# Performance work log

Measured on AMD Instinct MI355X. Metric: run time of the kernel, lower is better.

## Reference

```python
import jax, jax.numpy as jnp
import numpy as np

N_NODES, N_EDGES, N_FEAT, N_CLASSES = 100000, 1600000, 50, 40
K_HOPS = 2


def setup_inputs() -> dict:
    key = jax.random.key(0)
    k1, k2, k3 = jax.random.split(key, 3)
    x = jax.random.normal(k1, (N_NODES, N_FEAT), dtype=jnp.float32)
    edge_index = jax.random.randint(k2, (2, N_EDGES), 0, N_NODES, dtype=jnp.int64)
    # Linear(num_features -> num_classes) params (PyG stores [out,in]; we use [in,out])
    W = jax.random.normal(k3, (N_FEAT, N_CLASSES), dtype=jnp.float32) * 0.05
    b = jnp.zeros((N_CLASSES,), dtype=jnp.float32)
    return {"x": x, "edge_index": edge_index, "W": W, "b": b}


def reference(x, edge_index, W, b):
    N = x.shape[0]
    # gcn_norm: add self-loops, symmetric normalization D^-1/2 (A+I) D^-1/2
    loop = jnp.arange(N, dtype=edge_index.dtype)
    row = jnp.concatenate([edge_index[0], loop])  # source nodes
    col = jnp.concatenate([edge_index[1], loop])  # target nodes
    deg = jax.ops.segment_sum(jnp.ones(row.shape[0], x.dtype), col, num_segments=N)
    deg_inv_sqrt = jnp.where(deg > 0, jax.lax.rsqrt(deg), 0.0)
    norm = deg_inv_sqrt[row] * deg_inv_sqrt[col]  # [E+N]

    # K-hop propagation: h <- scatter_add(norm * h[row] -> col)
    h = x
    for _ in range(K_HOPS):
        h = jax.ops.segment_sum(norm[:, None] * h[row], col, num_segments=N)

    logits = h @ W + b  # [N, C]
    return jax.nn.log_softmax(logits, axis=1)
```

## Files before the change

kernel.cpp:

```cpp
#include <hip/hip_runtime.h>
#include <hip/hip_fp16.h>
#include <math.h>

#define NFEAT 50
#define NCLS 40
#define TPBK 256
#define TPBK_SHIFT 8
#define EPB 4096
#define MAXNB 512
#define CAP 8192

__device__ __forceinline__ __half2 u2h2(unsigned u) { return *(__half2*)&u; }
__device__ __forceinline__ unsigned h22u(__half2 h) { return *(unsigned*)&h; }
__device__ __forceinline__ __half2 shx_h2(__half2 v, int m) {
    int i = *(int*)&v; i = __shfl_xor(i, m); return *(__half2*)&i;
}


__global__ __launch_bounds__(1024) void k_bhist(const int* __restrict__ col, int E,
                                                int* __restrict__ hist, int NB) {
    __shared__ int h[MAXNB];
    for (int i = threadIdx.x; i < NB; i += 1024) h[i] = 0;
    __syncthreads();
    int i0 = blockIdx.x * EPB;
    #pragma unroll
    for (int k = 0; k < EPB / 1024; k++) {
        int e = i0 + k * 1024 + threadIdx.x;
        if (e < E) atomicAdd(&h[col[e] >> TPBK_SHIFT], 1);
    }
    __syncthreads();
    int* row = hist + (size_t)blockIdx.x * NB;
    for (int i = threadIdx.x; i < NB; i += 1024) row[i] = h[i];
}


__global__ __launch_bounds__(1024) void k_colscan(int* __restrict__ hist,
                                                  int* __restrict__ btot,
                                                  int NB, int PE) {
    int b = (blockIdx.x * 1024 + threadIdx.x) >> 6;
    int lane = threadIdx.x & 63;
    if (b >= NB) return;
    int carry = b * CAP;
    for (int c = 0; c < PE; c += 64) {
        int p = c + lane;
        int v = (p < PE) ? hist[(size_t)p * NB + b] : 0;
        int incl = v;
        #pragma unroll
        for (int d = 1; d < 64; d <<= 1) {
            int tmp = __shfl_up(incl, d);
            if (lane >= d) incl += tmp;
        }
        if (p < PE) hist[(size_t)p * NB + b] = carry + incl - v;
        carry += __shfl(incl, 63);
    }
    if (lane == 0) btot[b] = carry - b * CAP;
}


__global__ __launch_bounds__(1024) void k_part(const int* __restrict__ ei, int E,
                                               const int* __restrict__ hist,
                                               unsigned* __restrict__ pairs, int NB) {
    __shared__ int h[MAXNB];
    __shared__ int base[MAXNB];
    int t = threadIdx.x;
    const int* brow = hist + (size_t)blockIdx.x * NB;
    for (int i = t; i < NB; i += 1024) { h[i] = 0; base[i] = brow[i]; }
    __syncthreads();
    int i0 = blockIdx.x * EPB;
    int r[EPB / 1024], c[EPB / 1024];
    #pragma unroll
    for (int k = 0; k < EPB / 1024; k++) {
        int e = i0 + k * 1024 + t;
        if (e < E) {
            r[k] = ei[e];
            c[k] = ei[E + e];
        } else c[k] = -1;
    }
    #pragma unroll
    for (int k = 0; k < EPB / 1024; k++) {
        if (c[k] >= 0) {
            int bkt = c[k] >> TPBK_SHIFT;
            int p = base[bkt] + atomicAdd(&h[bkt], 1);
            pairs[p] = ((unsigned)r[k] << 8) | ((unsigned)c[k] & 255u);
        }
    }
}


__global__ __launch_bounds__(1024) void k_bucket(const unsigned* __restrict__ pairs,
                         const int* __restrict__ btot, int* __restrict__ rows,
                         int* __restrict__ cnt, int* __restrict__ offs,
                         float* __restrict__ dis, const float* __restrict__ x,
                         unsigned short* __restrict__ xb, int N) {
    int b = blockIdx.x;
    int ebeg = b * CAP, m = btot[b];
    int t0 = b << TPBK_SHIFT;
    __shared__ int h[TPBK];
    __shared__ int off[TPBK];
    __shared__ float diss[TPBK];
    __shared__ int wtot[4];
    int t = threadIdx.x;
    if (t < TPBK) h[t] = 0;
    __syncthreads();

    unsigned pc[4]; bool ok[4];
    #pragma unroll
    for (int k = 0; k < 4; k++) {
        int i = t + k * 1024;
        ok[k] = i < m;
        if (ok[k]) {
            pc[k] = pairs[ebeg + i];
            atomicAdd(&h[pc[k] & 255u], 1);
        }
    }
    for (int i = 4096 + t; i < m; i += 1024)
        atomicAdd(&h[pairs[ebeg + i] & 255u], 1);
    __syncthreads();

    int v = 0, incl = 0;
    if (t < TPBK) {
        v = h[t];
        h[t] = 0;
        incl = v;
        int l = t & 63;
        #pragma unroll
        for (int d = 1; d < 64; d <<= 1) {
            int tmp = __shfl_up(incl, d);
            if (l >= d) incl += tmp;
        }
        if (l == 63) wtot[t >> 6] = incl;
    }
    __syncthreads();
    if (t < TPBK) {
        int pre = 0;
        #pragma unroll
        for (int w = 0; w < 3; w++) if ((t >> 6) > w) pre += wtot[w];
        int excl = pre + incl - v;
        off[t] = excl;
        int tg = t0 + t;
        float d = rsqrtf((float)(v + 1));
        diss[t] = d;
        if (tg < N) {
            cnt[tg] = v;
            offs[tg] = ebeg + excl;
            dis[tg] = d;
        }
    }
    __syncthreads();

    #pragma unroll
    for (int k = 0; k < 4; k++) {
        if (ok[k]) {
            int lt = pc[k] & 255u;
            int pos = off[lt] + atomicAdd(&h[lt], 1);
            rows[ebeg + pos] = pc[k] >> 8;
        }
    }
    for (int i = 4096 + t; i < m; i += 1024) {
        unsigned p = pairs[ebeg + i];
        int lt = p & 255u;
        int pos = off[lt] + atomicAdd(&h[lt], 1);
        rows[ebeg + pos] = p >> 8;
    }

    int nmax = N - t0; if (nmax > TPBK) nmax = TPBK;
    for (int idx = t; idx < (nmax << 6); idx += 1024) {
        int nl = idx >> 6, f = idx & 63;
        int n = t0 + nl;
        float val = (f < NFEAT) ? x[(size_t)n * NFEAT + f] * diss[nl] : 0.f;
        __half hv = __float2half_rn(val);
        xb[((size_t)n << 6) + f] = *(unsigned short*)&hv;
    }
}


__global__ void k_prop(const unsigned short* __restrict__ zin, unsigned short* __restrict__ zout,
                       const float* __restrict__ dis, const int* __restrict__ offs,
                       const int* __restrict__ cnt, const int* __restrict__ rows, int N) {
    int wid = (blockIdx.x * blockDim.x + threadIdx.x) >> 6;
    int lane = threadIdx.x & 63;
    if (wid >= N) return;
    int g = lane >> 3;
    unsigned fl = (lane & 7) << 3;
    int beg = offs[wid], num = cnt[wid];

    uint4 sv = *(const uint4*)&zin[((unsigned)wid << 6) + fl];
    __half2 a0 = u2h2(g == 0 ? sv.x : 0u);
    __half2 a1 = u2h2(g == 0 ? sv.y : 0u);
    __half2 a2 = u2h2(g == 0 ? sv.z : 0u);
    __half2 a3 = u2h2(g == 0 ? sv.w : 0u);

    int full = num & ~31;
    int j = 0;
    for (; j < full; j += 32) {
        unsigned i0 = (unsigned)(beg + j) + (unsigned)g;
        int r0 = rows[i0], r1 = rows[i0 + 8], r2 = rows[i0 + 16], r3 = rows[i0 + 24];
        uint4 v0 = *(const uint4*)&zin[((unsigned)r0 << 6) + fl];
        uint4 v1 = *(const uint4*)&zin[((unsigned)r1 << 6) + fl];
        uint4 v2 = *(const uint4*)&zin[((unsigned)r2 << 6) + fl];
        uint4 v3 = *(const uint4*)&zin[((unsigned)r3 << 6) + fl];
        a0 = __hadd2(a0, __hadd2(__hadd2(u2h2(v0.x), u2h2(v1.x)),
                                 __hadd2(u2h2(v2.x), u2h2(v3.x))));
        a1 = __hadd2(a1, __hadd2(__hadd2(u2h2(v0.y), u2h2(v1.y)),
                                 __hadd2(u2h2(v2.y), u2h2(v3.y))));
        a2 = __hadd2(a2, __hadd2(__hadd2(u2h2(v0.z), u2h2(v1.z)),
                                 __hadd2(u2h2(v2.z), u2h2(v3.z))));
        a3 = __hadd2(a3, __hadd2(__hadd2(u2h2(v0.w), u2h2(v1.w)),
                                 __hadd2(u2h2(v2.w), u2h2(v3.w))));
    }
    if (j < num) {
        int e0 = j + g, e1 = e0 + 8, e2 = e0 + 16, e3 = e0 + 24;
        int c0 = e0 < num ? e0 : 0;
        int c1 = e1 < num ? e1 : 0;
        int c2 = e2 < num ? e2 : 0;
        int c3 = e3 < num ? e3 : 0;
        int r0 = rows[beg + c0];
        int r1 = rows[beg + c1];
        int r2 = rows[beg + c2];
        int r3 = rows[beg + c3];
        uint4 v0 = *(const uint4*)&zin[((unsigned)r0 << 6) + fl];
        uint4 v1 = *(const uint4*)&zin[((unsigned)r1 << 6) + fl];
        uint4 v2 = *(const uint4*)&zin[((unsigned)r2 << 6) + fl];
        uint4 v3 = *(const uint4*)&zin[((unsigned)r3 << 6) + fl];
        if (e0 >= num) { v0.x = 0u; v0.y = 0u; v0.z = 0u; v0.w = 0u; }
        if (e1 >= num) { v1.x = 0u; v1.y = 0u; v1.z = 0u; v1.w = 0u; }
        if (e2 >= num) { v2.x = 0u; v2.y = 0u; v2.z = 0u; v2.w = 0u; }
        if (e3 >= num) { v3.x = 0u; v3.y = 0u; v3.z = 0u; v3.w = 0u; }
        a0 = __hadd2(a0, __hadd2(__hadd2(u2h2(v0.x), u2h2(v1.x)),
                                 __hadd2(u2h2(v2.x), u2h2(v3.x))));
        a1 = __hadd2(a1, __hadd2(__hadd2(u2h2(v0.y), u2h2(v1.y)),
                                 __hadd2(u2h2(v2.y), u2h2(v3.y))));
        a2 = __hadd2(a2, __hadd2(__hadd2(u2h2(v0.z), u2h2(v1.z)),
                                 __hadd2(u2h2(v2.z), u2h2(v3.z))));
        a3 = __hadd2(a3, __hadd2(__hadd2(u2h2(v0.w), u2h2(v1.w)),
                                 __hadd2(u2h2(v2.w), u2h2(v3.w))));
    }

    a0 = __hadd2(a0, shx_h2(a0, 8)); a0 = __hadd2(a0, shx_h2(a0, 16)); a0 = __hadd2(a0, shx_h2(a0, 32));
    a1 = __hadd2(a1, shx_h2(a1, 8)); a1 = __hadd2(a1, shx_h2(a1, 16)); a1 = __hadd2(a1, shx_h2(a1, 32));
    a2 = __hadd2(a2, shx_h2(a2, 8)); a2 = __hadd2(a2, shx_h2(a2, 16)); a2 = __hadd2(a2, shx_h2(a2, 32));
    a3 = __hadd2(a3, shx_h2(a3, 8)); a3 = __hadd2(a3, shx_h2(a3, 16)); a3 = __hadd2(a3, shx_h2(a3, 32));

    if (lane < 8) {
        float dn = dis[wid];
        float s2 = dn * dn;
        float2 f0 = __half22float2(a0);
        float2 f1 = __half22float2(a1);
        float2 f2 = __half22float2(a2);
        float2 f3 = __half22float2(a3);
        uint4 o;
        o.x = h22u(__floats2half2_rn(f0.x * s2, f0.y * s2));
        o.y = h22u(__floats2half2_rn(f1.x * s2, f1.y * s2));
        o.z = h22u(__floats2half2_rn(f2.x * s2, f2.y * s2));
        o.w = h22u(__floats2half2_rn(f3.x * s2, f3.y * s2));
        *(uint4*)&zout[((unsigned)wid << 6) + fl] = o;
    }
}


__global__ void k_head(const unsigned short* __restrict__ z2, const int* __restrict__ cnt,
                       const float* __restrict__ W, const float* __restrict__ b,
                       float* __restrict__ out, int N) {
    int n = blockIdx.x * blockDim.x + threadIdx.x;
    if (n >= N) return;
    float s = sqrtf((float)(cnt[n] + 1));
    float acc[NCLS];
    #pragma unroll
    for (int c = 0; c < NCLS; c++) acc[c] = b[c];
    const unsigned* zr = (const unsigned*)&z2[(size_t)n << 6];
    #pragma unroll
    for (int k2 = 0; k2 < NFEAT / 2; k2++) {
        float2 hp = __half22float2(u2h2(zr[k2]));
        float h0 = hp.x * s, h1 = hp.y * s;
        #pragma unroll
        for (int c = 0; c < NCLS; c++)
            acc[c] += h0 * W[(2 * k2) * NCLS + c] + h1 * W[(2 * k2 + 1) * NCLS + c];
    }
    float m = acc[0];
    #pragma unroll
    for (int c = 1; c < NCLS; c++) m = fmaxf(m, acc[c]);
    float sum = 0.f;
    #pragma unroll
    for (int c = 0; c < NCLS; c++) sum += __expf(acc[c] - m);
    float l = __logf(sum) + m;
    #pragma unroll
    for (int c = 0; c < NCLS; c++) out[(size_t)n * NCLS + c] = acc[c] - l;
}


extern "C" void kernel_launch(void* const* d_in, const int* in_sizes, int n_in,
                              void* d_out, int out_size, void* d_ws, size_t ws_size,
                              hipStream_t stream) {
    const float* x = (const float*)d_in[0];
    const int* ei = (const int*)d_in[1];
    const float* W = (const float*)d_in[2];
    const float* b = (const float*)d_in[3];
    float* out = (float*)d_out;

    int N = in_sizes[0] / NFEAT;
    int E = in_sizes[1] / 2;
    int NB = (N + TPBK - 1) / TPBK;
    int pe = (E + EPB - 1) / EPB;

    char* w = (char*)d_ws;
    auto alloc = [&](size_t bytes) { char* p = w; w += (bytes + 255) & ~(size_t)255; return p; };
    int*   hist  = (int*)  alloc((size_t)pe * NB * 4);
    int*   btot  = (int*)  alloc((size_t)NB * 4);
    int*   cnt   = (int*)  alloc((size_t)N * 4);
    int*   offs  = (int*)  alloc((size_t)N * 4);
    float* dis   = (float*)alloc((size_t)N * 4);
    int*   rows  = (int*)  alloc((size_t)NB * CAP * 4);
    unsigned short* xb = (unsigned short*)alloc((size_t)N * 64 * 2);
    unsigned short* z1 = (unsigned short*)alloc((size_t)N * 64 * 2);
    size_t psz = (size_t)NB * CAP * 4, zsz = (size_t)N * 64 * 2;
    char* uni = alloc(psz > zsz ? psz : zsz);
    unsigned* pairs = (unsigned*)uni;
    unsigned short* z2 = (unsigned short*)uni;

    k_bhist<<<pe, 1024, 0, stream>>>(ei + E, E, hist, NB);
    int cb = (NB * 64 + 1023) / 1024;
    k_colscan<<<cb, 1024, 0, stream>>>(hist, btot, NB, pe);
    k_part<<<pe, 1024, 0, stream>>>(ei, E, hist, pairs, NB);
    k_bucket<<<NB, 1024, 0, stream>>>(pairs, btot, rows, cnt, offs, dis, x, xb, N);

    int pb = (int)(((size_t)N * 64 + 255) / 256);
    k_prop<<<pb, 256, 0, stream>>>(xb, z1, dis, offs, cnt, rows, N);
    k_prop<<<pb, 256, 0, stream>>>(z1, z2, dis, offs, cnt, rows, N);

    k_head<<<(N + 255) / 256, 256, 0, stream>>>(z2, cnt, W, b, out, N);
}
```

Baseline: 152.3 us.

## Split head GEMV+log_softmax across 8 lanes per node with shared-memory weights

The classifier head now assigns eight threads per node, each computing five classes, instead of one thread computing all forty. Weights and bias are staged into shared memory once per block. The softmax max and sum are reduced with xor shuffles across the eight lanes. This removes the 40-accumulator register pressure and the per-thread strided output writes, and makes better use of the GPU's parallelism. The cost is redundant loads of the node feature row by all eight lanes and the added shuffle reductions.

```diff
diff --git a/kernel.cpp b/kernel.cpp
--- a/kernel.cpp
+++ b/kernel.cpp
@@ -258,33 +258,58 @@
 }
 
 
-__global__ void k_head(const unsigned short* __restrict__ z2, const int* __restrict__ cnt,
+__global__ __launch_bounds__(256) void k_head(const unsigned short* __restrict__ z2,
+                       const int* __restrict__ cnt,
                        const float* __restrict__ W, const float* __restrict__ b,
                        float* __restrict__ out, int N) {
-    int n = blockIdx.x * blockDim.x + threadIdx.x;
+    __shared__ float Ws[NFEAT * NCLS];
+    __shared__ float bs[NCLS];
+    int t = threadIdx.x;
+    for (int i = t; i < NFEAT * NCLS / 4; i += 256)
+        *(float4*)&Ws[i * 4] = *(const float4*)&W[i * 4];
+    if (t < NCLS) bs[t] = b[t];
+    __syncthreads();
+
+    int tid = blockIdx.x * 256 + t;
+    int n = tid >> 3;
+    int l = tid & 7;
     if (n >= N) return;
-    float s = sqrtf((float)(cnt[n] + 1));
-    float acc[NCLS];
-    #pragma unroll
-    for (int c = 0; c < NCLS; c++) acc[c] = b[c];
+
+    float acc0 = 0.f, acc1 = 0.f, acc2 = 0.f, acc3 = 0.f, acc4 = 0.f;
     const unsigned* zr = (const unsigned*)&z2[(size_t)n << 6];
+    int cb = l * 5;
     #pragma unroll
     for (int k2 = 0; k2 < NFEAT / 2; k2++) {
         float2 hp = __half22float2(u2h2(zr[k2]));
-        float h0 = hp.x * s, h1 = hp.y * s;
-        #pragma unroll
-        for (int c = 0; c < NCLS; c++)
-            acc[c] += h0 * W[(2 * k2) * NCLS + c] + h1 * W[(2 * k2 + 1) * NCLS + c];
-    }
-    float m = acc[0];
-    #pragma unroll
-    for (int c = 1; c < NCLS; c++) m = fmaxf(m, acc[c]);
-    float sum = 0.f;
-    #pragma unroll
-    for (int c = 0; c < NCLS; c++) sum += __expf(acc[c] - m);
-    float l = __logf(sum) + m;
-    #pragma unroll
-    for (int c = 0; c < NCLS; c++) out[(size_t)n * NCLS + c] = acc[c] - l;
+        const float* w0 = &Ws[(2 * k2) * NCLS + cb];
+        const float* w1 = &Ws[(2 * k2 + 1) * NCLS + cb];
+        acc0 += hp.x * w0[0] + hp.y * w1[0];
+        acc1 += hp.x * w0[1] + hp.y * w1[1];
+        acc2 += hp.x * w0[2] + hp.y * w1[2];
+        acc3 += hp.x * w0[3] + hp.y * w1[3];
+        acc4 += hp.x * w0[4] + hp.y * w1[4];
+    }
+    float s = sqrtf((float)(cnt[n] + 1));
+    float l0 = s * acc0 + bs[cb + 0];
+    float l1 = s * acc1 + bs[cb + 1];
+    float l2 = s * acc2 + bs[cb + 2];
+    float l3 = s * acc3 + bs[cb + 3];
+    float l4 = s * acc4 + bs[cb + 4];
+
+    float m = fmaxf(fmaxf(fmaxf(l0, l1), fmaxf(l2, l3)), l4);
+    m = fmaxf(m, __shfl_xor(m, 1));
+    m = fmaxf(m, __shfl_xor(m, 2));
+    m = fmaxf(m, __shfl_xor(m, 4));
+    float sum = __expf(l0 - m) + __expf(l1 - m) + __expf(l2 - m)
+              + __expf(l3 - m) + __expf(l4 - m);
+    sum += __shfl_xor(sum, 1);
+    sum += __shfl_xor(sum, 2);
+    sum += __shfl_xor(sum, 4);
+    float lse = __logf(sum) + m;
+
+    float* o = &out[(size_t)n * NCLS + cb];
+    o[0] = l0 - lse; o[1] = l1 - lse; o[2] = l2 - lse;
+    o[3] = l3 - lse; o[4] = l4 - lse;
 }
 
 
@@ -327,5 +352,6 @@
     k_prop<<<pb, 256, 0, stream>>>(xb, z1, dis, offs, cnt, rows, N);
     k_prop<<<pb, 256, 0, stream>>>(z1, z2, dis, offs, cnt, rows, N);
 
-    k_head<<<(N + 255) / 256, 256, 0, stream>>>(z2, cnt, W, b, out, N);
-}
+    int hb = (int)(((size_t)N * 8 + 255) / 256);
+    k_head<<<hb, 256, 0, stream>>>(z2, cnt, W, b, out, N);
+}
```

Result: faster. 137.8 us (-9.5%).
